# Kernel optimization log

Measured on AMD Instinct MI355X. Metric: run time of the kernel, lower is better.

The kernel has to match this reference:

```python
import jax, jax.numpy as jnp
import numpy as np

HEADS = 4
DIM_HEAD = 64
QUERY_DIM = 512
CONTEXT_DIM = 512
INNER = HEADS * DIM_HEAD  # 256
SCALE = DIM_HEAD ** -0.5


def setup_inputs() -> dict:
    key = jax.random.key(0)
    ks = jax.random.split(key, 9)
    b, n, m = 4, 2048, 2048
    inp = {
        'x1': jax.random.normal(ks[0], (b, n, QUERY_DIM), jnp.float32),
        'x2': jax.random.normal(ks[1], (b, n, QUERY_DIM), jnp.float32),
        'context': jax.random.normal(ks[2], (b, m, CONTEXT_DIM), jnp.float32),
        # weights stored [in, out] (= torch weight.T)
        'Wq': jax.random.normal(ks[3], (QUERY_DIM, INNER), jnp.float32) * (QUERY_DIM ** -0.5),
        'Wq2': jax.random.normal(ks[4], (QUERY_DIM, INNER), jnp.float32) * (QUERY_DIM ** -0.5),
        'Wk': jax.random.normal(ks[5], (CONTEXT_DIM, INNER), jnp.float32) * (CONTEXT_DIM ** -0.5),
        'Wv': jax.random.normal(ks[6], (CONTEXT_DIM, INNER), jnp.float32) * (CONTEXT_DIM ** -0.5),
        'Wo': jax.random.normal(ks[7], (INNER, QUERY_DIM), jnp.float32) * (INNER ** -0.5),
        'bo': jax.random.normal(ks[8], (QUERY_DIM,), jnp.float32) * 0.01,
    }
    return inp


def _split_heads(t):
    # [b, n, h*d] -> [b, h, n, d]
    b, n, _ = t.shape
    return t.reshape(b, n, HEADS, DIM_HEAD).transpose(0, 2, 1, 3)


def reference(x1, x2, context, Wq, Wq2, Wk, Wv, Wo, bo):
    q = _split_heads(x1 @ Wq)
    q2 = _split_heads(x2 @ Wq2)
    k = _split_heads(context @ Wk)
    v = _split_heads(context @ Wv)
    sim = jnp.einsum('bhid,bhjd->bhij', q, k) * SCALE
    sim2 = jnp.einsum('bhid,bhjd->bhij', q2, k) * SCALE
    attn = 0.3 * jax.nn.softmax(sim, axis=-1) + 0.7 * jax.nn.softmax(sim2, axis=-1)
    out = jnp.einsum('bhij,bhjd->bhid', attn, v)  # [b, h, n, d]
    b, h, n, d = out.shape
    out = out.transpose(0, 2, 1, 3).reshape(b, n, h * d)
    return out @ Wo + bo
```

## Files before the change

kernel.cpp:

```cpp
#include <hip/hip_runtime.h>

typedef __attribute__((ext_vector_type(8))) short bf16x8;
typedef __attribute__((ext_vector_type(4))) float f32x4;
typedef unsigned short ushort_t;
typedef unsigned int uint_t;

__device__ __forceinline__ ushort_t f2bf(float f) {
    return __builtin_bit_cast(ushort_t, (__bf16)f);
}
__device__ __forceinline__ uint_t pack2(float a, float b) {
    return (uint_t)f2bf(a) | ((uint_t)f2bf(b) << 16);
}

#define LOG2E 1.4426950408889634f

#define WT_OFF   0
#define WOT_OFF  524288
#define QKV_OFF  655360
#define QKV_SZ   2097152
#define QKV_OFF_Z3 (3 * (size_t)QKV_SZ)
#define O_OFF    9043968

__global__ __launch_bounds__(256) void transpose_w(
    const float* __restrict__ Wq, const float* __restrict__ Wq2,
    const float* __restrict__ Wk, const float* __restrict__ Wv,
    const float* __restrict__ Wo, ushort_t* __restrict__ ws)
{
    __shared__ ushort_t lT[64][72];
    const int j = blockIdx.y;
    const int bx = blockIdx.x;
    const float* in;
    ushort_t* out;
    int C;
    if (j < 4) {
        in = (j == 0) ? Wq : (j == 1) ? Wq2 : (j == 2) ? Wk : Wv;
        out = ws + WT_OFF + (size_t)j * 131072; C = 256;
    } else {
        in = Wo; out = ws + WOT_OFF; C = 512;
    }
    const int R = 131072 / C;
    const int tc = C >> 6;
    const int r0 = (bx / tc) * 64, c0 = (bx % tc) * 64;
    const int t = threadIdx.x;
    const int ir = t >> 4, ic = (t & 15) * 4;
#pragma unroll
    for (int i = 0; i < 4; ++i) {
        const int r = ir + i * 16;
        float4 v = *(const float4*)(in + (size_t)(r0 + r) * C + c0 + ic);
        uint2 w; w.x = pack2(v.x, v.y); w.y = pack2(v.z, v.w);
        *(uint2*)&lT[r][ic] = w;
    }
    __syncthreads();
    const int oc = t >> 2, rr0 = (t & 3) * 16;
    ushort_t g[16];
#pragma unroll
    for (int k = 0; k < 16; ++k) g[k] = lT[rr0 + k][oc];
    ushort_t* op = out + (size_t)(c0 + oc) * R + r0 + rr0;
    *(uint4*)op = *(const uint4*)&g[0];
    *(uint4*)(op + 8) = *(const uint4*)&g[8];
}

#define PROJ_STAGE(K0, BUF) do {                                                     \
    _Pragma("unroll")                                                                \
    for (int it_ = 0; it_ < 4; ++it_) {                                              \
        const int p_ = tid + it_ * 256;                                              \
        const ushort_t* bp_ = Bt + (size_t)(p_ >> 2) * 512 + (K0) + ((p_ & 3) << 3); \
        __builtin_amdgcn_global_load_lds(                                            \
            (const __attribute__((address_space(1))) void*)bp_,                      \
            (__attribute__((address_space(3))) void*)&lB[BUF][p_ * 8], 16, 0, 0);    \
    }                                                                                \
} while (0)

__global__ __launch_bounds__(256) void proj_gemm(
    const float* __restrict__ x1, const float* __restrict__ x2,
    const float* __restrict__ ctx, const ushort_t* __restrict__ Wt,
    ushort_t* __restrict__ QKV)
{
    __shared__ __align__(16) ushort_t lB[2][256 * 32];
    const int z = blockIdx.y;
    const float* A = (z == 0) ? x1 : (z == 1) ? x2 : ctx;
    const ushort_t* Bt = Wt + (size_t)z * 131072;
    const float sc = (z < 2) ? (0.125f * LOG2E) : 1.0f;
    const int tid = threadIdx.x;
    const int wave = tid >> 6, lane = tid & 63;
    const int quad = lane >> 4, l16 = lane & 15;
    const size_t row0 = (size_t)blockIdx.x * 64;

    PROJ_STAGE(0, 0);

    const float* arow = A + (row0 + wave * 16 + l16) * 512 + quad * 8;
    float4 a0 = *(const float4*)(arow);
    float4 a1 = *(const float4*)(arow + 4);

    f32x4 acc[16] = {};
    for (int k0 = 0; k0 < 512; k0 += 32) {
        const int pb = (k0 >> 5) & 1;
        __syncthreads();
        if (k0 + 32 < 512) PROJ_STAGE(k0 + 32, 1 - pb);
        float4 n0 = a0, n1 = a1;
        if (k0 + 32 < 512) {
            n0 = *(const float4*)(arow + k0 + 32);
            n1 = *(const float4*)(arow + k0 + 36);
        }
        uint4 aw;
        aw.x = pack2(a0.x, a0.y); aw.y = pack2(a0.z, a0.w);
        aw.z = pack2(a1.x, a1.y); aw.w = pack2(a1.z, a1.w);
        bf16x8 af = __builtin_bit_cast(bf16x8, aw);
#pragma unroll
        for (int c = 0; c < 16; ++c) {
            bf16x8 bfr = *(const bf16x8*)&lB[pb][(c * 16 + l16) * 32 + quad * 8];
            acc[c] = __builtin_amdgcn_mfma_f32_16x16x32_bf16(af, bfr, acc[c], 0, 0, 0);
        }
        a0 = n0; a1 = n1;
    }

    if (z == 3) {
        const int b = (int)(row0 >> 11);
        const int tokl = ((int)row0 & 2047) + wave * 16 + quad * 4;
        ushort_t* Vt = QKV + QKV_OFF_Z3;
#pragma unroll
        for (int c = 0; c < 16; ++c) {
            const int col = c * 16 + l16;
            const int h = col >> 6, d = col & 63;
            uint2 w;
            w.x = pack2(acc[c][0], acc[c][1]);
            w.y = pack2(acc[c][2], acc[c][3]);
            *(uint2*)(Vt + ((size_t)((b * 4 + h) * 64 + d)) * 2048 + tokl) = w;
        }
    } else {
        ushort_t* C = QKV + (size_t)z * QKV_SZ;
#pragma unroll
        for (int c = 0; c < 16; ++c) {
            const int col = c * 16 + l16;
#pragma unroll
            for (int r = 0; r < 4; ++r)
                C[(row0 + wave * 16 + quad * 4 + r) * 256 + col] = f2bf(acc[c][r] * sc);
        }
    }
}

#define OUT_STAGE(K0, BUF) do {                                                      \
    _Pragma("unroll")                                                                \
    for (int it_ = 0; it_ < 2; ++it_) {                                              \
        const int p_ = tid + it_ * 256;                                              \
        const ushort_t* bp_ = Wot + (size_t)(col0 + (p_ >> 2)) * 256 + (K0) + ((p_ & 3) << 3); \
        __builtin_amdgcn_global_load_lds(                                            \
            (const __attribute__((address_space(1))) void*)bp_,                      \
            (__attribute__((address_space(3))) void*)&lB[BUF][p_ * 8], 16, 0, 0);    \
    }                                                                                \
} while (0)

__global__ __launch_bounds__(256) void out_gemm(
    const ushort_t* __restrict__ Op, const ushort_t* __restrict__ Wot,
    const float* __restrict__ bias, float* __restrict__ out)
{
    __shared__ __align__(16) ushort_t lB[2][128 * 32];
    const int tid = threadIdx.x;
    const int wave = tid >> 6, lane = tid & 63;
    const int quad = lane >> 4, l16 = lane & 15;
    const size_t row0 = (size_t)blockIdx.x * 64;
    const int col0 = blockIdx.y * 128;

    OUT_STAGE(0, 0);
    const ushort_t* arow = Op + (row0 + wave * 16 + l16) * 256 + quad * 8;
    bf16x8 af = *(const bf16x8*)(arow);

    f32x4 acc[8] = {};
    for (int k0 = 0; k0 < 256; k0 += 32) {
        const int pb = (k0 >> 5) & 1;
        __syncthreads();
        if (k0 + 32 < 256) OUT_STAGE(k0 + 32, 1 - pb);
        bf16x8 an = af;
        if (k0 + 32 < 256) an = *(const bf16x8*)(arow + k0 + 32);
#pragma unroll
        for (int c = 0; c < 8; ++c) {
            bf16x8 bfr = *(const bf16x8*)&lB[pb][(c * 16 + l16) * 32 + quad * 8];
            acc[c] = __builtin_amdgcn_mfma_f32_16x16x32_bf16(af, bfr, acc[c], 0, 0, 0);
        }
        af = an;
    }
#pragma unroll
    for (int c = 0; c < 8; ++c) {
        const int col = col0 + c * 16 + l16;
        const float bv = bias[col];
#pragma unroll
        for (int r = 0; r < 4; ++r)
            out[(row0 + wave * 16 + quad * 4 + r) * 512 + col] = acc[c][r] + bv;
    }
}


#define ATTN_STAGE(MB, BUF) do {                                                        \
    _Pragma("unroll")                                                                   \
    for (int it_ = 0; it_ < 2; ++it_) {                                                 \
        const int cc_ = tid + it_ * 256;                                                \
        const int g_ = (cc_ ^ (cc_ >> 3)) & 7;                                          \
        const ushort_t* kp_ = Kb + (size_t)(tok0 + (MB) + (cc_ >> 3)) * 256 + in0 + g_ * 8; \
        __builtin_amdgcn_global_load_lds(                                               \
            (const __attribute__((address_space(1))) void*)kp_,                         \
            (__attribute__((address_space(3))) void*)&lK[BUF][cc_ * 8], 16, 0, 0);      \
        const ushort_t* vp_ = Vt + (size_t)(bh64 + (cc_ >> 3)) * 2048 + (MB) + g_ * 8;  \
        __builtin_amdgcn_global_load_lds(                                               \
            (const __attribute__((address_space(1))) void*)vp_,                         \
            (__attribute__((address_space(3))) void*)&lV[BUF][cc_ * 8], 16, 0, 0);      \
    }                                                                                   \
} while (0)

#define ATTN_ITER(I, P) do {                                                            \
    __syncthreads();                                                                    \
    { const int mn_ = ((I) + 1) * 64; if (mn_ < 2048) ATTN_STAGE(mn_, 1 - (P)); }       \
    f32x4 st1[4] = {}, st2[4] = {};                                                     \
    _Pragma("unroll")                                                                   \
    for (int c = 0; c < 4; ++c) {                                                       \
        _Pragma("unroll")                                                               \
        for (int ks = 0; ks < 2; ++ks) {                                                \
            bf16x8 kf = *(const bf16x8*)&lK[P][(c * 16 + l16) * 64 +                    \
                                              ((((ks * 4 + quad) ^ l7) & 7) << 3)];     \
            st1[c] = __builtin_amdgcn_mfma_f32_16x16x32_bf16(kf, q1f[ks], st1[c], 0, 0, 0); \
            st2[c] = __builtin_amdgcn_mfma_f32_16x16x32_bf16(kf, q2f[ks], st2[c], 0, 0, 0); \
        } }                                                                             \
    _Pragma("unroll")                                                                   \
    for (int c = 0; c < 4; ++c) {                                                       \
        float p0 = __builtin_amdgcn_exp2f(st1[c][0]);                                   \
        float p1 = __builtin_amdgcn_exp2f(st1[c][1]);                                   \
        float p2 = __builtin_amdgcn_exp2f(st1[c][2]);                                   \
        float p3 = __builtin_amdgcn_exp2f(st1[c][3]);                                   \
        l1 += (p0 + p1) + (p2 + p3);                                                    \
        uint2 w; w.x = pack2(p0, p1); w.y = pack2(p2, p3);                              \
        *(uint2*)&lPw0[l16 * 72 + c * 16 + quad * 4] = w;                               \
        float r0 = __builtin_amdgcn_exp2f(st2[c][0]);                                   \
        float r1 = __builtin_amdgcn_exp2f(st2[c][1]);                                   \
        float r2 = __builtin_amdgcn_exp2f(st2[c][2]);                                   \
        float r3 = __builtin_amdgcn_exp2f(st2[c][3]);                                   \
        l2 += (r0 + r1) + (r2 + r3);                                                    \
        uint2 y; y.x = pack2(r0, r1); y.y = pack2(r2, r3);                              \
        *(uint2*)&lPw1[l16 * 72 + c * 16 + quad * 4] = y;                               \
    }                                                                                   \
    bf16x8 pa1[2], pa2[2];                                                              \
    _Pragma("unroll")                                                                   \
    for (int ks = 0; ks < 2; ++ks) {                                                    \
        pa1[ks] = *(const bf16x8*)&lPw0[l16 * 72 + ks * 32 + quad * 8];                 \
        pa2[ks] = *(const bf16x8*)&lPw1[l16 * 72 + ks * 32 + quad * 8];                 \
    }                                                                                   \
    _Pragma("unroll")                                                                   \
    for (int c = 0; c < 4; ++c) {                                                       \
        _Pragma("unroll")                                                               \
        for (int ks = 0; ks < 2; ++ks) {                                                \
            bf16x8 vf = *(const bf16x8*)&lV[P][(c * 16 + l16) * 64 +                    \
                                              ((((ks * 4 + quad) ^ l7) & 7) << 3)];     \
            o1[c] = __builtin_amdgcn_mfma_f32_16x16x32_bf16(vf, pa1[ks], o1[c], 0, 0, 0); \
            o2[c] = __builtin_amdgcn_mfma_f32_16x16x32_bf16(vf, pa2[ks], o2[c], 0, 0, 0); \
        } }                                                                             \
} while (0)

__global__ __launch_bounds__(256) void attn_fused(
    const ushort_t* __restrict__ Qb, const ushort_t* __restrict__ Q2b,
    const ushort_t* __restrict__ Kb, const ushort_t* __restrict__ Vt,
    ushort_t* __restrict__ Ob)
{
    __shared__ __align__(16) ushort_t lK[2][64 * 64];
    __shared__ __align__(16) ushort_t lV[2][64 * 64];
    __shared__ __align__(16) ushort_t lP[4][2][16 * 72];

    const int qt = blockIdx.x;
    const int bh = blockIdx.y;
    const int tid = threadIdx.x;
    const int wave = tid >> 6, lane = tid & 63;
    const int quad = lane >> 4, l16 = lane & 15;
    const int l7 = l16 & 7;
    const size_t tok0 = (size_t)(bh >> 2) * 2048;
    const int in0 = (bh & 3) * 64;
    const int bh64 = bh * 64;
    ushort_t* lPw0 = &lP[wave][0][0];
    ushort_t* lPw1 = &lP[wave][1][0];

    bf16x8 q1f[2], q2f[2];
    {
        const ushort_t* qr1 = Qb  + (tok0 + qt * 64 + wave * 16 + l16) * 256 + in0;
        const ushort_t* qr2 = Q2b + (tok0 + qt * 64 + wave * 16 + l16) * 256 + in0;
#pragma unroll
        for (int ks = 0; ks < 2; ++ks) {
            q1f[ks] = *(const bf16x8*)(qr1 + ks * 32 + quad * 8);
            q2f[ks] = *(const bf16x8*)(qr2 + ks * 32 + quad * 8);
        }
    }

    ATTN_STAGE(0, 0);

    f32x4 o1[4] = {}, o2[4] = {};
    float l1 = 0.f, l2 = 0.f;

    for (int i = 0; i < 32; i += 2) {
        ATTN_ITER(i, 0);
        ATTN_ITER(i + 1, 1);
    }

    l1 += __shfl_xor(l1, 16, 64); l1 += __shfl_xor(l1, 32, 64);
    l2 += __shfl_xor(l2, 16, 64); l2 += __shfl_xor(l2, 32, 64);
    const float inv1 = 0.3f / l1, inv2 = 0.7f / l2;

    ushort_t* orow = Ob + (tok0 + qt * 64 + wave * 16 + l16) * 256 + in0;
#pragma unroll
    for (int c = 0; c < 4; ++c) {
        const float f0 = o1[c][0] * inv1 + o2[c][0] * inv2;
        const float f1 = o1[c][1] * inv1 + o2[c][1] * inv2;
        const float f2 = o1[c][2] * inv1 + o2[c][2] * inv2;
        const float f3 = o1[c][3] * inv1 + o2[c][3] * inv2;
        uint2 w; w.x = pack2(f0, f1); w.y = pack2(f2, f3);
        *(uint2*)(orow + c * 16 + quad * 4) = w;
    }
}

extern "C" void kernel_launch(void* const* d_in, const int* in_sizes, int n_in,
                              void* d_out, int out_size, void* d_ws, size_t ws_size,
                              hipStream_t stream)
{
    (void)in_sizes; (void)n_in; (void)out_size; (void)ws_size;
    const float* x1  = (const float*)d_in[0];
    const float* x2  = (const float*)d_in[1];
    const float* ctx = (const float*)d_in[2];
    const float* Wq  = (const float*)d_in[3];
    const float* Wq2 = (const float*)d_in[4];
    const float* Wk  = (const float*)d_in[5];
    const float* Wv  = (const float*)d_in[6];
    const float* Wo  = (const float*)d_in[7];
    const float* bo  = (const float*)d_in[8];
    ushort_t* ws  = (ushort_t*)d_ws;
    float* out = (float*)d_out;

    ushort_t* Wt  = ws + WT_OFF;
    ushort_t* Wot = ws + WOT_OFF;
    ushort_t* QKV = ws + QKV_OFF;
    ushort_t* Q   = QKV;
    ushort_t* Q2  = QKV + 1 * (size_t)QKV_SZ;
    ushort_t* Kp  = QKV + 2 * (size_t)QKV_SZ;
    ushort_t* Vt  = QKV + 3 * (size_t)QKV_SZ;
    ushort_t* Op  = ws + O_OFF;

    transpose_w<<<dim3(32, 5),  256, 0, stream>>>(Wq, Wq2, Wk, Wv, Wo, ws);
    proj_gemm  <<<dim3(128, 4), 256, 0, stream>>>(x1, x2, ctx, Wt, QKV);
    attn_fused <<<dim3(32, 16), 256, 0, stream>>>(Q, Q2, Kp, Vt, Op);
    out_gemm   <<<dim3(128, 4), 256, 0, stream>>>(Op, Wot, bo, out);
}
```

Baseline: 182.2 us.

## Use 2x2 wave tiling in projection and output GEMMs

Changes the warp layout in proj_gemm and out_gemm from four waves each covering 16 rows by all columns to a 2x2 arrangement. Each wave now covers 32 rows by half the columns. Each LDS B fragment feeds two MFMAs, which halves LDS reads of B per MFMA. The cost is that each wave loads twice as many A rows from global memory and converts them, and neighbouring waves duplicate those loads.

```diff
diff --git a/kernel.cpp b/kernel.cpp
--- a/kernel.cpp
+++ b/kernel.cpp
@@ -84,57 +84,73 @@
     const int tid = threadIdx.x;
     const int wave = tid >> 6, lane = tid & 63;
     const int quad = lane >> 4, l16 = lane & 15;
+    const int wr = wave >> 1, wc = wave & 1;
     const size_t row0 = (size_t)blockIdx.x * 64;
 
     PROJ_STAGE(0, 0);
 
-    const float* arow = A + (row0 + wave * 16 + l16) * 512 + quad * 8;
-    float4 a0 = *(const float4*)(arow);
-    float4 a1 = *(const float4*)(arow + 4);
-
-    f32x4 acc[16] = {};
+    const float* arow0 = A + (row0 + wr * 32 + l16) * 512 + quad * 8;
+    const float* arow1 = arow0 + 16 * 512;
+    float4 a00 = *(const float4*)(arow0);
+    float4 a01 = *(const float4*)(arow0 + 4);
+    float4 a10 = *(const float4*)(arow1);
+    float4 a11 = *(const float4*)(arow1 + 4);
+
+    f32x4 acc[8][2] = {};
     for (int k0 = 0; k0 < 512; k0 += 32) {
         const int pb = (k0 >> 5) & 1;
         __syncthreads();
         if (k0 + 32 < 512) PROJ_STAGE(k0 + 32, 1 - pb);
-        float4 n0 = a0, n1 = a1;
+        float4 n00 = a00, n01 = a01, n10 = a10, n11 = a11;
         if (k0 + 32 < 512) {
-            n0 = *(const float4*)(arow + k0 + 32);
-            n1 = *(const float4*)(arow + k0 + 36);
-        }
-        uint4 aw;
-        aw.x = pack2(a0.x, a0.y); aw.y = pack2(a0.z, a0.w);
-        aw.z = pack2(a1.x, a1.y); aw.w = pack2(a1.z, a1.w);
-        bf16x8 af = __builtin_bit_cast(bf16x8, aw);
-#pragma unroll
-        for (int c = 0; c < 16; ++c) {
-            bf16x8 bfr = *(const bf16x8*)&lB[pb][(c * 16 + l16) * 32 + quad * 8];
-            acc[c] = __builtin_amdgcn_mfma_f32_16x16x32_bf16(af, bfr, acc[c], 0, 0, 0);
-        }
-        a0 = n0; a1 = n1;
+            n00 = *(const float4*)(arow0 + k0 + 32);
+            n01 = *(const float4*)(arow0 + k0 + 36);
+            n10 = *(const float4*)(arow1 + k0 + 32);
+            n11 = *(const float4*)(arow1 + k0 + 36);
+        }
+        uint4 aw0, aw1;
+        aw0.x = pack2(a00.x, a00.y); aw0.y = pack2(a00.z, a00.w);
+        aw0.z = pack2(a01.x, a01.y); aw0.w = pack2(a01.z, a01.w);
+        aw1.x = pack2(a10.x, a10.y); aw1.y = pack2(a10.z, a10.w);
+        aw1.z = pack2(a11.x, a11.y); aw1.w = pack2(a11.z, a11.w);
+        bf16x8 af0 = __builtin_bit_cast(bf16x8, aw0);
+        bf16x8 af1 = __builtin_bit_cast(bf16x8, aw1);
+#pragma unroll
+        for (int c = 0; c < 8; ++c) {
+            bf16x8 bfr = *(const bf16x8*)&lB[pb][((wc * 8 + c) * 16 + l16) * 32 + quad * 8];
+            acc[c][0] = __builtin_amdgcn_mfma_f32_16x16x32_bf16(af0, bfr, acc[c][0], 0, 0, 0);
+            acc[c][1] = __builtin_amdgcn_mfma_f32_16x16x32_bf16(af1, bfr, acc[c][1], 0, 0, 0);
+        }
+        a00 = n00; a01 = n01; a10 = n10; a11 = n11;
     }
 
     if (z == 3) {
         const int b = (int)(row0 >> 11);
-        const int tokl = ((int)row0 & 2047) + wave * 16 + quad * 4;
         ushort_t* Vt = QKV + QKV_OFF_Z3;
 #pragma unroll
-        for (int c = 0; c < 16; ++c) {
-            const int col = c * 16 + l16;
+        for (int c = 0; c < 8; ++c) {
+            const int col = wc * 128 + c * 16 + l16;
             const int h = col >> 6, d = col & 63;
-            uint2 w;
-            w.x = pack2(acc[c][0], acc[c][1]);
-            w.y = pack2(acc[c][2], acc[c][3]);
-            *(uint2*)(Vt + ((size_t)((b * 4 + h) * 64 + d)) * 2048 + tokl) = w;
+#pragma unroll
+            for (int rg = 0; rg < 2; ++rg) {
+                const int tokl = ((int)row0 & 2047) + wr * 32 + rg * 16 + quad * 4;
+                uint2 w;
+                w.x = pack2(acc[c][rg][0], acc[c][rg][1]);
+                w.y = pack2(acc[c][rg][2], acc[c][rg][3]);
+                *(uint2*)(Vt + ((size_t)((b * 4 + h) * 64 + d)) * 2048 + tokl) = w;
+            }
         }
     } else {
         ushort_t* C = QKV + (size_t)z * QKV_SZ;
 #pragma unroll
-        for (int c = 0; c < 16; ++c) {
-            const int col = c * 16 + l16;
-#pragma unroll
-            for (int r = 0; r < 4; ++r)
-                C[(row0 + wave * 16 + quad * 4 + r) * 256 + col] = f2bf(acc[c][r] * sc);
+        for (int c = 0; c < 8; ++c) {
+            const int col = wc * 128 + c * 16 + l16;
+#pragma unroll
+            for (int rg = 0; rg < 2; ++rg)
+#pragma unroll
+                for (int r = 0; r < 4; ++r)
+                    C[(row0 + wr * 32 + rg * 16 + quad * 4 + r) * 256 + col] =
+                        f2bf(acc[c][rg][r] * sc);
         }
     }
 }
@@ -158,34 +174,44 @@
     const int tid = threadIdx.x;
     const int wave = tid >> 6, lane = tid & 63;
     const int quad = lane >> 4, l16 = lane & 15;
+    const int wr = wave >> 1, wc = wave & 1;
     const size_t row0 = (size_t)blockIdx.x * 64;
     const int col0 = blockIdx.y * 128;
 
     OUT_STAGE(0, 0);
-    const ushort_t* arow = Op + (row0 + wave * 16 + l16) * 256 + quad * 8;
-    bf16x8 af = *(const bf16x8*)(arow);
-
-    f32x4 acc[8] = {};
+    const ushort_t* arow0 = Op + (row0 + wr * 32 + l16) * 256 + quad * 8;
+    const ushort_t* arow1 = arow0 + 16 * 256;
+    bf16x8 af0 = *(const bf16x8*)(arow0);
+    bf16x8 af1 = *(const bf16x8*)(arow1);
+
+    f32x4 acc[4][2] = {};
     for (int k0 = 0; k0 < 256; k0 += 32) {
         const int pb = (k0 >> 5) & 1;
         __syncthreads();
         if (k0 + 32 < 256) OUT_STAGE(k0 + 32, 1 - pb);
-        bf16x8 an = af;
-        if (k0 + 32 < 256) an = *(const bf16x8*)(arow + k0 + 32);
-#pragma unroll
-        for (int c = 0; c < 8; ++c) {
-            bf16x8 bfr = *(const bf16x8*)&lB[pb][(c * 16 + l16) * 32 + quad * 8];
-            acc[c] = __builtin_amdgcn_mfma_f32_16x16x32_bf16(af, bfr, acc[c], 0, 0, 0);
-        }
-        af = an;
-    }
-#pragma unroll
-    for (int c = 0; c < 8; ++c) {
-        const int col = col0 + c * 16 + l16;
+        bf16x8 an0 = af0, an1 = af1;
+        if (k0 + 32 < 256) {
+            an0 = *(const bf16x8*)(arow0 + k0 + 32);
+            an1 = *(const bf16x8*)(arow1 + k0 + 32);
+        }
+#pragma unroll
+        for (int c = 0; c < 4; ++c) {
+            bf16x8 bfr = *(const bf16x8*)&lB[pb][((wc * 4 + c) * 16 + l16) * 32 + quad * 8];
+            acc[c][0] = __builtin_amdgcn_mfma_f32_16x16x32_bf16(af0, bfr, acc[c][0], 0, 0, 0);
+            acc[c][1] = __builtin_amdgcn_mfma_f32_16x16x32_bf16(af1, bfr, acc[c][1], 0, 0, 0);
+        }
+        af0 = an0; af1 = an1;
+    }
+#pragma unroll
+    for (int c = 0; c < 4; ++c) {
+        const int col = col0 + wc * 64 + c * 16 + l16;
         const float bv = bias[col];
 #pragma unroll
-        for (int r = 0; r < 4; ++r)
-            out[(row0 + wave * 16 + quad * 4 + r) * 512 + col] = acc[c][r] + bv;
+        for (int rg = 0; rg < 2; ++rg)
+#pragma unroll
+            for (int r = 0; r < 4; ++r)
+                out[(row0 + wr * 32 + rg * 16 + quad * 4 + r) * 512 + col] =
+                    acc[c][rg][r] + bv;
     }
 }
 
```

After: 190.5 us. 1.05x slower.

## Software-pipeline attention: overlap PV MFMAs of previous tile with current QK softmax

Applied to the files above, without the earlier changes.

Restructures the attention loop so the P·V matrix multiplies for the previous key tile run after the current tile's QK^T MFMAs and before its exp/softmax work. This is meant to let MFMA work overlap the transcendental and LDS-store latency of the softmax stage. To keep the previous tile's V resident, the K/V shared-memory buffers go from double to triple buffering with rotating pointers, which raises LDS use from 32KB to 48KB for K/V and may lower occupancy. Runtime pointer rotation also replaces the compile-time buffer indices, which can add address arithmetic.

```diff
diff --git a/kernel.cpp b/kernel.cpp
--- a/kernel.cpp
+++ b/kernel.cpp
@@ -190,7 +190,7 @@
 }
 
 
-#define ATTN_STAGE(MB, BUF) do {                                                        \
+#define ATTN_STAGE(MB, KDST, VDST) do {                                                 \
     _Pragma("unroll")                                                                   \
     for (int it_ = 0; it_ < 2; ++it_) {                                                 \
         const int cc_ = tid + it_ * 256;                                                \
@@ -198,59 +198,12 @@
         const ushort_t* kp_ = Kb + (size_t)(tok0 + (MB) + (cc_ >> 3)) * 256 + in0 + g_ * 8; \
         __builtin_amdgcn_global_load_lds(                                               \
             (const __attribute__((address_space(1))) void*)kp_,                         \
-            (__attribute__((address_space(3))) void*)&lK[BUF][cc_ * 8], 16, 0, 0);      \
+            (__attribute__((address_space(3))) void*)&(KDST)[cc_ * 8], 16, 0, 0);       \
         const ushort_t* vp_ = Vt + (size_t)(bh64 + (cc_ >> 3)) * 2048 + (MB) + g_ * 8;  \
         __builtin_amdgcn_global_load_lds(                                               \
             (const __attribute__((address_space(1))) void*)vp_,                         \
-            (__attribute__((address_space(3))) void*)&lV[BUF][cc_ * 8], 16, 0, 0);      \
+            (__attribute__((address_space(3))) void*)&(VDST)[cc_ * 8], 16, 0, 0);       \
     }                                                                                   \
-} while (0)
-
-#define ATTN_ITER(I, P) do {                                                            \
-    __syncthreads();                                                                    \
-    { const int mn_ = ((I) + 1) * 64; if (mn_ < 2048) ATTN_STAGE(mn_, 1 - (P)); }       \
-    f32x4 st1[4] = {}, st2[4] = {};                                                     \
-    _Pragma("unroll")                                                                   \
-    for (int c = 0; c < 4; ++c) {                                                       \
-        _Pragma("unroll")                                                               \
-        for (int ks = 0; ks < 2; ++ks) {                                                \
-            bf16x8 kf = *(const bf16x8*)&lK[P][(c * 16 + l16) * 64 +                    \
-                                              ((((ks * 4 + quad) ^ l7) & 7) << 3)];     \
-            st1[c] = __builtin_amdgcn_mfma_f32_16x16x32_bf16(kf, q1f[ks], st1[c], 0, 0, 0); \
-            st2[c] = __builtin_amdgcn_mfma_f32_16x16x32_bf16(kf, q2f[ks], st2[c], 0, 0, 0); \
-        } }                                                                             \
-    _Pragma("unroll")                                                                   \
-    for (int c = 0; c < 4; ++c) {                                                       \
-        float p0 = __builtin_amdgcn_exp2f(st1[c][0]);                                   \
-        float p1 = __builtin_amdgcn_exp2f(st1[c][1]);                                   \
-        float p2 = __builtin_amdgcn_exp2f(st1[c][2]);                                   \
-        float p3 = __builtin_amdgcn_exp2f(st1[c][3]);                                   \
-        l1 += (p0 + p1) + (p2 + p3);                                                    \
-        uint2 w; w.x = pack2(p0, p1); w.y = pack2(p2, p3);                              \
-        *(uint2*)&lPw0[l16 * 72 + c * 16 + quad * 4] = w;                               \
-        float r0 = __builtin_amdgcn_exp2f(st2[c][0]);                                   \
-        float r1 = __builtin_amdgcn_exp2f(st2[c][1]);                                   \
-        float r2 = __builtin_amdgcn_exp2f(st2[c][2]);                                   \
-        float r3 = __builtin_amdgcn_exp2f(st2[c][3]);                                   \
-        l2 += (r0 + r1) + (r2 + r3);                                                    \
-        uint2 y; y.x = pack2(r0, r1); y.y = pack2(r2, r3);                              \
-        *(uint2*)&lPw1[l16 * 72 + c * 16 + quad * 4] = y;                               \
-    }                                                                                   \
-    bf16x8 pa1[2], pa2[2];                                                              \
-    _Pragma("unroll")                                                                   \
-    for (int ks = 0; ks < 2; ++ks) {                                                    \
-        pa1[ks] = *(const bf16x8*)&lPw0[l16 * 72 + ks * 32 + quad * 8];                 \
-        pa2[ks] = *(const bf16x8*)&lPw1[l16 * 72 + ks * 32 + quad * 8];                 \
-    }                                                                                   \
-    _Pragma("unroll")                                                                   \
-    for (int c = 0; c < 4; ++c) {                                                       \
-        _Pragma("unroll")                                                               \
-        for (int ks = 0; ks < 2; ++ks) {                                                \
-            bf16x8 vf = *(const bf16x8*)&lV[P][(c * 16 + l16) * 64 +                    \
-                                              ((((ks * 4 + quad) ^ l7) & 7) << 3)];     \
-            o1[c] = __builtin_amdgcn_mfma_f32_16x16x32_bf16(vf, pa1[ks], o1[c], 0, 0, 0); \
-            o2[c] = __builtin_amdgcn_mfma_f32_16x16x32_bf16(vf, pa2[ks], o2[c], 0, 0, 0); \
-        } }                                                                             \
 } while (0)
 
 __global__ __launch_bounds__(256) void attn_fused(
@@ -258,8 +211,8 @@
     const ushort_t* __restrict__ Kb, const ushort_t* __restrict__ Vt,
     ushort_t* __restrict__ Ob)
 {
-    __shared__ __align__(16) ushort_t lK[2][64 * 64];
-    __shared__ __align__(16) ushort_t lV[2][64 * 64];
+    __shared__ __align__(16) ushort_t lK[3][64 * 64];
+    __shared__ __align__(16) ushort_t lV[3][64 * 64];
     __shared__ __align__(16) ushort_t lP[4][2][16 * 72];
 
     const int qt = blockIdx.x;
@@ -285,14 +238,81 @@
         }
     }
 
-    ATTN_STAGE(0, 0);
+    ushort_t* pKcur = &lK[0][0]; ushort_t* pVcur = &lV[0][0];
+    ushort_t* pKpre = &lK[1][0]; ushort_t* pVpre = &lV[1][0];
+    ushort_t* pKold = &lK[2][0]; ushort_t* pVold = &lV[2][0];
+
+    ATTN_STAGE(0, pKcur, pVcur);
 
     f32x4 o1[4] = {}, o2[4] = {};
+    bf16x8 pa1[2], pa2[2];
     float l1 = 0.f, l2 = 0.f;
 
-    for (int i = 0; i < 32; i += 2) {
-        ATTN_ITER(i, 0);
-        ATTN_ITER(i + 1, 1);
+    for (int i = 0; i < 32; ++i) {
+        __syncthreads();
+        if (i < 31) ATTN_STAGE((i + 1) * 64, pKpre, pVpre);
+
+        f32x4 st1[4] = {}, st2[4] = {};
+#pragma unroll
+        for (int c = 0; c < 4; ++c) {
+#pragma unroll
+            for (int ks = 0; ks < 2; ++ks) {
+                bf16x8 kf = *(const bf16x8*)&pKcur[(c * 16 + l16) * 64 +
+                                                   ((((ks * 4 + quad) ^ l7) & 7) << 3)];
+                st1[c] = __builtin_amdgcn_mfma_f32_16x16x32_bf16(kf, q1f[ks], st1[c], 0, 0, 0);
+                st2[c] = __builtin_amdgcn_mfma_f32_16x16x32_bf16(kf, q2f[ks], st2[c], 0, 0, 0);
+            }
+        }
+
+        if (i > 0) {
+#pragma unroll
+            for (int c = 0; c < 4; ++c) {
+#pragma unroll
+                for (int ks = 0; ks < 2; ++ks) {
+                    bf16x8 vf = *(const bf16x8*)&pVold[(c * 16 + l16) * 64 +
+                                                       ((((ks * 4 + quad) ^ l7) & 7) << 3)];
+                    o1[c] = __builtin_amdgcn_mfma_f32_16x16x32_bf16(vf, pa1[ks], o1[c], 0, 0, 0);
+                    o2[c] = __builtin_amdgcn_mfma_f32_16x16x32_bf16(vf, pa2[ks], o2[c], 0, 0, 0);
+                }
+            }
+        }
+
+#pragma unroll
+        for (int c = 0; c < 4; ++c) {
+            float p0 = __builtin_amdgcn_exp2f(st1[c][0]);
+            float p1 = __builtin_amdgcn_exp2f(st1[c][1]);
+            float p2 = __builtin_amdgcn_exp2f(st1[c][2]);
+            float p3 = __builtin_amdgcn_exp2f(st1[c][3]);
+            l1 += (p0 + p1) + (p2 + p3);
+            uint2 w; w.x = pack2(p0, p1); w.y = pack2(p2, p3);
+            *(uint2*)&lPw0[l16 * 72 + c * 16 + quad * 4] = w;
+            float r0 = __builtin_amdgcn_exp2f(st2[c][0]);
+            float r1 = __builtin_amdgcn_exp2f(st2[c][1]);
+            float r2 = __builtin_amdgcn_exp2f(st2[c][2]);
+            float r3 = __builtin_amdgcn_exp2f(st2[c][3]);
+            l2 += (r0 + r1) + (r2 + r3);
+            uint2 y; y.x = pack2(r0, r1); y.y = pack2(r2, r3);
+            *(uint2*)&lPw1[l16 * 72 + c * 16 + quad * 4] = y;
+        }
+#pragma unroll
+        for (int ks = 0; ks < 2; ++ks) {
+            pa1[ks] = *(const bf16x8*)&lPw0[l16 * 72 + ks * 32 + quad * 8];
+            pa2[ks] = *(const bf16x8*)&lPw1[l16 * 72 + ks * 32 + quad * 8];
+        }
+
+        ushort_t* tK = pKold; pKold = pKcur; pKcur = pKpre; pKpre = tK;
+        ushort_t* tV = pVold; pVold = pVcur; pVcur = pVpre; pVpre = tV;
+    }
+
+#pragma unroll
+    for (int c = 0; c < 4; ++c) {
+#pragma unroll
+        for (int ks = 0; ks < 2; ++ks) {
+            bf16x8 vf = *(const bf16x8*)&pVold[(c * 16 + l16) * 64 +
+                                               ((((ks * 4 + quad) ^ l7) & 7) << 3)];
+            o1[c] = __builtin_amdgcn_mfma_f32_16x16x32_bf16(vf, pa1[ks], o1[c], 0, 0, 0);
+            o2[c] = __builtin_amdgcn_mfma_f32_16x16x32_bf16(vf, pa2[ks], o2[c], 0, 0, 0);
+        }
     }
 
     l1 += __shfl_xor(l1, 16, 64); l1 += __shfl_xor(l1, 32, 64);
```

New measurement: 176.0 us. -3.4%, faster.

## Load K/V fragments directly from global memory and software-pipeline PV with next QK

Applied to the files above, without the earlier changes.

Drops the LDS double-buffered K/V staging and its block-wide barriers; each wave now reads K and V MFMA fragments straight from global memory (relying on L1/L2 for reuse across the four waves). The loop is also reordered so the PV multiply of tile i-1 is issued before the QK/softmax of tile i, to overlap work. This removes the syncthreads and LDS traffic but makes every wave fetch the full K/V tiles itself, so global/cache bandwidth and load latency may become the bottleneck.

```diff
diff --git a/kernel.cpp b/kernel.cpp
--- a/kernel.cpp
+++ b/kernel.cpp
@@ -190,34 +190,20 @@
 }
 
 
-#define ATTN_STAGE(MB, BUF) do {                                                        \
-    _Pragma("unroll")                                                                   \
-    for (int it_ = 0; it_ < 2; ++it_) {                                                 \
-        const int cc_ = tid + it_ * 256;                                                \
-        const int g_ = (cc_ ^ (cc_ >> 3)) & 7;                                          \
-        const ushort_t* kp_ = Kb + (size_t)(tok0 + (MB) + (cc_ >> 3)) * 256 + in0 + g_ * 8; \
-        __builtin_amdgcn_global_load_lds(                                               \
-            (const __attribute__((address_space(1))) void*)kp_,                         \
-            (__attribute__((address_space(3))) void*)&lK[BUF][cc_ * 8], 16, 0, 0);      \
-        const ushort_t* vp_ = Vt + (size_t)(bh64 + (cc_ >> 3)) * 2048 + (MB) + g_ * 8;  \
-        __builtin_amdgcn_global_load_lds(                                               \
-            (const __attribute__((address_space(1))) void*)vp_,                         \
-            (__attribute__((address_space(3))) void*)&lV[BUF][cc_ * 8], 16, 0, 0);      \
-    }                                                                                   \
-} while (0)
-
-#define ATTN_ITER(I, P) do {                                                            \
-    __syncthreads();                                                                    \
-    { const int mn_ = ((I) + 1) * 64; if (mn_ < 2048) ATTN_STAGE(mn_, 1 - (P)); }       \
+#define ATTN_QK_SM(I) do {                                                              \
+    bf16x8 kf[4][2];                                                                    \
+    _Pragma("unroll")                                                                   \
+    for (int c = 0; c < 4; ++c)                                                         \
+        _Pragma("unroll")                                                               \
+        for (int ks = 0; ks < 2; ++ks)                                                  \
+            kf[c][ks] = *(const bf16x8*)(Kbase + (size_t)((I) * 64 + c * 16) * 256 + ks * 32); \
     f32x4 st1[4] = {}, st2[4] = {};                                                     \
     _Pragma("unroll")                                                                   \
     for (int c = 0; c < 4; ++c) {                                                       \
         _Pragma("unroll")                                                               \
         for (int ks = 0; ks < 2; ++ks) {                                                \
-            bf16x8 kf = *(const bf16x8*)&lK[P][(c * 16 + l16) * 64 +                    \
-                                              ((((ks * 4 + quad) ^ l7) & 7) << 3)];     \
-            st1[c] = __builtin_amdgcn_mfma_f32_16x16x32_bf16(kf, q1f[ks], st1[c], 0, 0, 0); \
-            st2[c] = __builtin_amdgcn_mfma_f32_16x16x32_bf16(kf, q2f[ks], st2[c], 0, 0, 0); \
+            st1[c] = __builtin_amdgcn_mfma_f32_16x16x32_bf16(kf[c][ks], q1f[ks], st1[c], 0, 0, 0); \
+            st2[c] = __builtin_amdgcn_mfma_f32_16x16x32_bf16(kf[c][ks], q2f[ks], st2[c], 0, 0, 0); \
         } }                                                                             \
     _Pragma("unroll")                                                                   \
     for (int c = 0; c < 4; ++c) {                                                       \
@@ -236,18 +222,19 @@
         uint2 y; y.x = pack2(r0, r1); y.y = pack2(r2, r3);                              \
         *(uint2*)&lPw1[l16 * 72 + c * 16 + quad * 4] = y;                               \
     }                                                                                   \
-    bf16x8 pa1[2], pa2[2];                                                              \
     _Pragma("unroll")                                                                   \
     for (int ks = 0; ks < 2; ++ks) {                                                    \
         pa1[ks] = *(const bf16x8*)&lPw0[l16 * 72 + ks * 32 + quad * 8];                 \
         pa2[ks] = *(const bf16x8*)&lPw1[l16 * 72 + ks * 32 + quad * 8];                 \
     }                                                                                   \
+} while (0)
+
+#define ATTN_PV(I) do {                                                                 \
     _Pragma("unroll")                                                                   \
     for (int c = 0; c < 4; ++c) {                                                       \
         _Pragma("unroll")                                                               \
         for (int ks = 0; ks < 2; ++ks) {                                                \
-            bf16x8 vf = *(const bf16x8*)&lV[P][(c * 16 + l16) * 64 +                    \
-                                              ((((ks * 4 + quad) ^ l7) & 7) << 3)];     \
+            bf16x8 vf = *(const bf16x8*)(Vbase + (size_t)(c * 16) * 2048 + (I) * 64 + ks * 32); \
             o1[c] = __builtin_amdgcn_mfma_f32_16x16x32_bf16(vf, pa1[ks], o1[c], 0, 0, 0); \
             o2[c] = __builtin_amdgcn_mfma_f32_16x16x32_bf16(vf, pa2[ks], o2[c], 0, 0, 0); \
         } }                                                                             \
@@ -258,8 +245,6 @@
     const ushort_t* __restrict__ Kb, const ushort_t* __restrict__ Vt,
     ushort_t* __restrict__ Ob)
 {
-    __shared__ __align__(16) ushort_t lK[2][64 * 64];
-    __shared__ __align__(16) ushort_t lV[2][64 * 64];
     __shared__ __align__(16) ushort_t lP[4][2][16 * 72];
 
     const int qt = blockIdx.x;
@@ -267,7 +252,6 @@
     const int tid = threadIdx.x;
     const int wave = tid >> 6, lane = tid & 63;
     const int quad = lane >> 4, l16 = lane & 15;
-    const int l7 = l16 & 7;
     const size_t tok0 = (size_t)(bh >> 2) * 2048;
     const int in0 = (bh & 3) * 64;
     const int bh64 = bh * 64;
@@ -285,15 +269,19 @@
         }
     }
 
-    ATTN_STAGE(0, 0);
+    const ushort_t* Kbase = Kb + (tok0 + l16) * 256 + in0 + quad * 8;
+    const ushort_t* Vbase = Vt + ((size_t)(bh64 + l16)) * 2048 + quad * 8;
 
     f32x4 o1[4] = {}, o2[4] = {};
+    bf16x8 pa1[2], pa2[2];
     float l1 = 0.f, l2 = 0.f;
 
-    for (int i = 0; i < 32; i += 2) {
-        ATTN_ITER(i, 0);
-        ATTN_ITER(i + 1, 1);
-    }
+    ATTN_QK_SM(0);
+    for (int i = 1; i < 32; ++i) {
+        ATTN_PV(i - 1);
+        ATTN_QK_SM(i);
+    }
+    ATTN_PV(31);
 
     l1 += __shfl_xor(l1, 16, 64); l1 += __shfl_xor(l1, 32, 64);
     l2 += __shfl_xor(l2, 16, 64); l2 += __shfl_xor(l2, 32, 64);
```

Result: slower. 258.2 us (+41.8%).
